# Kernel tuning notes

Hardware: AMD Instinct MI355X
Metric: run time of the kernel (lower is better)

## Reference

```python
import jax, jax.numpy as jnp
import numpy as np

N_HEADS = 16
D_HEAD = 64
QUERY_DIM = 1024
CONTEXT_DIM = 1024
INNER = N_HEADS * D_HEAD


def setup_inputs() -> dict:
    key = jax.random.key(0)
    ks = jax.random.split(key, 7)
    B, Nq, Nk = 4, 1024, 1024
    x = jax.random.normal(ks[0], (B, Nq, QUERY_DIM), dtype=jnp.float32)
    context = jax.random.normal(ks[1], (B, Nk, CONTEXT_DIM), dtype=jnp.float32)
    s_q = 1.0 / np.sqrt(QUERY_DIM)
    s_c = 1.0 / np.sqrt(CONTEXT_DIM)
    s_i = 1.0 / np.sqrt(INNER)
    Wq = jax.random.uniform(ks[2], (QUERY_DIM, INNER), jnp.float32, -s_q, s_q)
    Wk = jax.random.uniform(ks[3], (CONTEXT_DIM, INNER), jnp.float32, -s_c, s_c)
    Wv = jax.random.uniform(ks[4], (CONTEXT_DIM, INNER), jnp.float32, -s_c, s_c)
    Wo = jax.random.uniform(ks[5], (INNER, QUERY_DIM), jnp.float32, -s_i, s_i)
    bo = jax.random.uniform(ks[6], (QUERY_DIM,), jnp.float32, -s_i, s_i)
    return {"x": x, "context": context, "Wq": Wq, "Wk": Wk, "Wv": Wv, "Wo": Wo, "bo": bo}


def reference(x, context, Wq, Wk, Wv, Wo, bo):
    B, Nq, _ = x.shape
    Nk = context.shape[1]
    scale = D_HEAD ** -0.5
    # project and split heads: [B, H, N, d]
    q = (x @ Wq).reshape(B, Nq, N_HEADS, D_HEAD).transpose(0, 2, 1, 3)
    k = (context @ Wk).reshape(B, Nk, N_HEADS, D_HEAD).transpose(0, 2, 1, 3)
    v = (context @ Wv).reshape(B, Nk, N_HEADS, D_HEAD).transpose(0, 2, 1, 3)
    scores = jnp.einsum("bhqd,bhkd->bhqk", q, k) * scale
    attn = jax.nn.softmax(scores, axis=-1)
    out = jnp.einsum("bhqk,bhkd->bhqd", attn, v)
    out = out.transpose(0, 2, 1, 3).reshape(B, Nq, INNER)
    return out @ Wo + bo
```

## Files before the change

### kernel.cpp

```cpp
#include <hip/hip_runtime.h>
#include <hip/hip_bf16.h>

#define BATCH 4
#define NQ 1024
#define NKK 1024
#define HD 1024
#define NHEADS 16

typedef __bf16 bf16x8 __attribute__((ext_vector_type(8)));
typedef float f32x4 __attribute__((ext_vector_type(4)));
typedef unsigned short u16;
typedef unsigned int u32;

__device__ __forceinline__ u16 f2bf(float f) {
    union { __bf16 h; u16 u; } v;
    v.h = (__bf16)f;
    return v.u;
}

#define GLOAD16(gp, lp) \
    __builtin_amdgcn_global_load_lds((const __attribute__((address_space(1))) void*)(gp), \
                                     (__attribute__((address_space(3))) void*)(lp), 16, 0, 0)

#define MFMA16(a, b, c) __builtin_amdgcn_mfma_f32_16x16x32_bf16(a, b, c, 0, 0, 0)

__global__ __launch_bounds__(256) void cvt2bf_k(const float* __restrict__ a,
                                                u16* __restrict__ o, int n4) {
    int i = blockIdx.x * blockDim.x + threadIdx.x;
    const int stride = gridDim.x * blockDim.x;
    for (; i < n4; i += stride) {
        float4 v = ((const float4*)a)[i];
        ushort4 p;
        p.x = f2bf(v.x); p.y = f2bf(v.y); p.z = f2bf(v.z); p.w = f2bf(v.w);
        ((ushort4*)o)[i] = p;
    }
}

__global__ __launch_bounds__(256) void transpose4_k(const float* __restrict__ w0,
                                                    const float* __restrict__ w1,
                                                    const float* __restrict__ w2,
                                                    const float* __restrict__ w3,
                                                    u16* __restrict__ ws) {
    const float* src = blockIdx.z == 0 ? w0 : blockIdx.z == 1 ? w1 : blockIdx.z == 2 ? w2 : w3;
    const float scl = (blockIdx.z == 0) ? 0.18033688011112042f : 1.0f;
    u16* dst = ws + (size_t)blockIdx.z * (1024u * 1024u);
    __shared__ u16 t[64][65];
    const int bx = blockIdx.x * 64;
    const int by = blockIdx.y * 64;
    const int tid = threadIdx.x;
#pragma unroll
    for (int p = 0; p < 16; ++p) {
        int idx = p * 256 + tid;
        int r = idx >> 6, c = idx & 63;
        t[c][r] = f2bf(scl * src[(size_t)(by + r) * 1024 + bx + c]);
    }
    __syncthreads();
#pragma unroll
    for (int p = 0; p < 16; ++p) {
        int idx = p * 256 + tid;
        int r = idx >> 6, c = idx & 63;
        dst[(size_t)(bx + r) * 1024 + by + c] = t[r][c];
    }
}

__global__ __launch_bounds__(256) void gemm_qkv(const u16* __restrict__ Xb,
                                                const u16* __restrict__ Cb,
                                                const u16* __restrict__ WqT,
                                                const u16* __restrict__ WkT,
                                                const u16* __restrict__ WvT,
                                                u16* __restrict__ Qb,
                                                u16* __restrict__ Kb,
                                                u16* __restrict__ VTb) {
    const int bid = blockIdx.x;
    const int swz = (bid & 7) * 192 + (bid >> 3);
    const int z = swz / 512;
    const int rem = swz - z * 512;
    const int m0 = (rem >> 3) * 64;
    const int n0 = (rem & 7) * 128;

    const u16* __restrict__ A  = (z == 0) ? Xb : Cb;
    const u16* __restrict__ BT = (z == 0) ? WqT : (z == 1) ? WkT : WvT;

    __shared__ __align__(16) u16 Asm[64 * 64];
    __shared__ __align__(16) u16 Bsm[128 * 64];

    const int tid = threadIdx.x, lane = tid & 63, wv = tid >> 6;
    const int wm = wv >> 1, wn = wv & 1;
    const int lr = lane & 15, lg = lane >> 4;
    const int lx = lr & 7;
    const int M = BATCH * NQ, N = HD, K = HD;

    f32x4 acc[2][4];
#pragma unroll
    for (int i = 0; i < 2; ++i)
#pragma unroll
        for (int j = 0; j < 4; ++j) acc[i][j] = (f32x4)(0.0f);

    for (int kt = 0; kt < K; kt += 64) {
        __syncthreads();
#pragma unroll
        for (int i = 0; i < 2; ++i) {
            const int cb = (wv * 2 + i) * 64;
            const int s = cb + lane;
            const int row = s >> 3, cg = (s & 7) ^ (row & 7);
            GLOAD16(A + (size_t)(m0 + row) * K + kt + cg * 8, &Asm[cb * 8]);
        }
#pragma unroll
        for (int i = 0; i < 4; ++i) {
            const int cb = (wv * 4 + i) * 64;
            const int s = cb + lane;
            const int row = s >> 3, cg = (s & 7) ^ (row & 7);
            GLOAD16(BT + (size_t)(n0 + row) * K + kt + cg * 8, &Bsm[cb * 8]);
        }
        __syncthreads();
        bf16x8 af[2][2], bfr[4][2];
#pragma unroll
        for (int m = 0; m < 2; ++m)
#pragma unroll
            for (int kk = 0; kk < 2; ++kk)
                af[m][kk] = *(const bf16x8*)&Asm[((wm * 32 + m * 16 + lr) * 8 +
                                                 ((kk * 4 + lg) ^ lx)) * 8];
#pragma unroll
        for (int n = 0; n < 4; ++n)
#pragma unroll
            for (int kk = 0; kk < 2; ++kk)
                bfr[n][kk] = *(const bf16x8*)&Bsm[((wn * 64 + n * 16 + lr) * 8 +
                                                  ((kk * 4 + lg) ^ lx)) * 8];
#pragma unroll
        for (int kk = 0; kk < 2; ++kk)
#pragma unroll
            for (int m = 0; m < 2; ++m)
#pragma unroll
                for (int n = 0; n < 4; ++n)
                    acc[m][n] = MFMA16(af[m][kk], bfr[n][kk], acc[m][n]);
    }

    if (z < 2) {
        u16* __restrict__ C = (z == 0) ? Qb : Kb;
#pragma unroll
        for (int m = 0; m < 2; ++m)
#pragma unroll
            for (int n = 0; n < 4; ++n) {
                const int col = n0 + wn * 64 + n * 16 + lr;
                const int rb = m0 + wm * 32 + m * 16 + lg * 4;
#pragma unroll
                for (int r = 0; r < 4; ++r)
                    C[(size_t)(rb + r) * N + col] = f2bf(acc[m][n][r]);
            }
    } else {
#pragma unroll
        for (int m = 0; m < 2; ++m)
#pragma unroll
            for (int n = 0; n < 4; ++n) {
                const int col = n0 + wn * 64 + n * 16 + lr;
                const int rb = m0 + wm * 32 + m * 16 + lg * 4;
                ushort4 pk;
                pk.x = f2bf(acc[m][n][0]);
                pk.y = f2bf(acc[m][n][1]);
                pk.z = f2bf(acc[m][n][2]);
                pk.w = f2bf(acc[m][n][3]);
                *(ushort4*)&VTb[(size_t)col * M + rb] = pk;
            }
    }
}

__global__ __launch_bounds__(256) void gemm_out(const u16* __restrict__ A,
                                                const u16* __restrict__ BT,
                                                const float* __restrict__ bias,
                                                float* __restrict__ C) {
    const int bid = blockIdx.x;
    const int swz = (bid & 7) * 64 + (bid >> 3);
    const int m0 = (swz >> 3) * 64;
    const int n0 = (swz & 7) * 128;

    __shared__ __align__(16) u16 Asm[64 * 64];
    __shared__ __align__(16) u16 Bsm[128 * 64];

    const int tid = threadIdx.x, lane = tid & 63, wv = tid >> 6;
    const int wm = wv >> 1, wn = wv & 1;
    const int lr = lane & 15, lg = lane >> 4;
    const int lx = lr & 7;
    const int N = HD, K = HD;

    f32x4 acc[2][4];
#pragma unroll
    for (int i = 0; i < 2; ++i)
#pragma unroll
        for (int j = 0; j < 4; ++j) acc[i][j] = (f32x4)(0.0f);

    for (int kt = 0; kt < K; kt += 64) {
        __syncthreads();
#pragma unroll
        for (int i = 0; i < 2; ++i) {
            const int cb = (wv * 2 + i) * 64;
            const int s = cb + lane;
            const int row = s >> 3, cg = (s & 7) ^ (row & 7);
            GLOAD16(A + (size_t)(m0 + row) * K + kt + cg * 8, &Asm[cb * 8]);
        }
#pragma unroll
        for (int i = 0; i < 4; ++i) {
            const int cb = (wv * 4 + i) * 64;
            const int s = cb + lane;
            const int row = s >> 3, cg = (s & 7) ^ (row & 7);
            GLOAD16(BT + (size_t)(n0 + row) * K + kt + cg * 8, &Bsm[cb * 8]);
        }
        __syncthreads();
        bf16x8 af[2][2], bfr[4][2];
#pragma unroll
        for (int m = 0; m < 2; ++m)
#pragma unroll
            for (int kk = 0; kk < 2; ++kk)
                af[m][kk] = *(const bf16x8*)&Asm[((wm * 32 + m * 16 + lr) * 8 +
                                                 ((kk * 4 + lg) ^ lx)) * 8];
#pragma unroll
        for (int n = 0; n < 4; ++n)
#pragma unroll
            for (int kk = 0; kk < 2; ++kk)
                bfr[n][kk] = *(const bf16x8*)&Bsm[((wn * 64 + n * 16 + lr) * 8 +
                                                  ((kk * 4 + lg) ^ lx)) * 8];
#pragma unroll
        for (int kk = 0; kk < 2; ++kk)
#pragma unroll
            for (int m = 0; m < 2; ++m)
#pragma unroll
                for (int n = 0; n < 4; ++n)
                    acc[m][n] = MFMA16(af[m][kk], bfr[n][kk], acc[m][n]);
    }

#pragma unroll
    for (int m = 0; m < 2; ++m)
#pragma unroll
        for (int n = 0; n < 4; ++n) {
            const int col = n0 + wn * 64 + n * 16 + lr;
            const int rb = m0 + wm * 32 + m * 16 + lg * 4;
            const float bv = bias[col];
#pragma unroll
            for (int r = 0; r < 4; ++r)
                C[(size_t)(rb + r) * N + col] = acc[m][n][r] + bv;
        }
}

__global__ __launch_bounds__(256) void attn_k(const u16* __restrict__ Q,
                                              const u16* __restrict__ Kp,
                                              const u16* __restrict__ VT,
                                              u16* __restrict__ AO) {
    __shared__ __align__(16) u16 Ksm[2][64 * 64];
    __shared__ __align__(16) u16 Vsm[2][64 * 64];
    __shared__ __align__(16) u16 Psm[4][16 * 64];

    const int tid = threadIdx.x, lane = tid & 63, wv = tid >> 6;
    const int lr = lane & 15, lg = lane >> 4;

    const int swz = (blockIdx.x & 7) * 128 + (blockIdx.x >> 3);
    const int bh = swz >> 4;
    const int b = bh >> 4, h = bh & 15;
    const int q0 = (swz & 15) * 64 + wv * 16;
    const int lx = lr & 7;

    bf16x8 qf[2];
#pragma unroll
    for (int ks = 0; ks < 2; ++ks)
        qf[ks] = *(const bf16x8*)&Q[(size_t)(b * NQ + q0 + lr) * HD +
                                    h * 64 + ks * 32 + lg * 8];

    const int kbase = b * NKK, vrow0 = h * 64;
    auto stageKV = [&](int kt, int bufsel) {
#pragma unroll
        for (int i = 0; i < 2; ++i) {
            const int cb = (wv * 2 + i) * 64;
            const int s = cb + lane;
            const int row = s >> 3;
            const int cg = (s & 7) ^ (row & 7);
            GLOAD16(Kp + (size_t)(kbase + kt + row) * HD + h * 64 + cg * 8,
                    &Ksm[bufsel][cb * 8]);
            GLOAD16(VT + (size_t)(vrow0 + row) * (BATCH * NKK) + kbase + kt + cg * 8,
                    &Vsm[bufsel][cb * 8]);
        }
    };

    float sum = 0.0f;
    f32x4 o[4];
#pragma unroll
    for (int n = 0; n < 4; ++n) o[n] = (f32x4)(0.0f);

    stageKV(0, 0);
    __syncthreads();
    int cur = 0;

    for (int t = 0; t < NKK / 64; ++t) {
        if (t + 1 < NKK / 64) stageKV((t + 1) * 64, cur ^ 1);
        const u16* Ks = &Ksm[cur][0];
        const u16* Vs = &Vsm[cur][0];

        f32x4 s[4];
#pragma unroll
        for (int n = 0; n < 4; ++n) s[n] = (f32x4)(0.0f);
        __builtin_amdgcn_s_setprio(1);
#pragma unroll
        for (int n = 0; n < 4; ++n) {
            bf16x8 kf0 = *(const bf16x8*)&Ks[(n * 16 + lr) * 64 + (lg ^ lx) * 8];
            bf16x8 kf1 = *(const bf16x8*)&Ks[(n * 16 + lr) * 64 + ((lg | 4) ^ lx) * 8];
            s[n] = MFMA16(kf0, qf[0], s[n]);
            s[n] = MFMA16(kf1, qf[1], s[n]);
        }
        __builtin_amdgcn_s_setprio(0);

        u16* P = &Psm[wv][0];
#pragma unroll
        for (int n = 0; n < 4; ++n) {
            const float p0 = exp2f(s[n][0]);
            const float p1 = exp2f(s[n][1]);
            const float p2 = exp2f(s[n][2]);
            const float p3 = exp2f(s[n][3]);
            sum += (p0 + p1) + (p2 + p3);
            ushort4 pk;
            pk.x = f2bf(p0); pk.y = f2bf(p1); pk.z = f2bf(p2); pk.w = f2bf(p3);
            const int ch = (2 * n + (lg >> 1)) ^ lx;
            *(ushort4*)&P[lr * 64 + ch * 8 + (lg & 1) * 4] = pk;
        }

#pragma unroll
        for (int ks = 0; ks < 2; ++ks) {
            bf16x8 pa = *(const bf16x8*)&P[lr * 64 + (((ks * 4 + lg) ^ lx)) * 8];
            __builtin_amdgcn_s_setprio(1);
#pragma unroll
            for (int n = 0; n < 4; ++n) {
                bf16x8 vf = *(const bf16x8*)&Vs[(n * 16 + lr) * 64 + (((ks * 4 + lg) ^ lx)) * 8];
                o[n] = MFMA16(pa, vf, o[n]);
            }
            __builtin_amdgcn_s_setprio(0);
        }
        __syncthreads();
        cur ^= 1;
    }

    float v = sum;
    v += __shfl_xor(v, 16);
    v += __shfl_xor(v, 32);
    float rs[4];
#pragma unroll
    for (int r = 0; r < 4; ++r)
        rs[r] = 1.0f / __shfl(v, lg * 4 + r);

#pragma unroll
    for (int n = 0; n < 4; ++n)
#pragma unroll
        for (int r = 0; r < 4; ++r) {
            const float val = o[n][r] * rs[r];
            AO[(size_t)(b * NQ + q0 + lg * 4 + r) * HD +
               h * 64 + n * 16 + lr] = f2bf(val);
        }
}

extern "C" void kernel_launch(void* const* d_in, const int* in_sizes, int n_in,
                              void* d_out, int out_size, void* d_ws, size_t ws_size,
                              hipStream_t stream) {
    const float* x   = (const float*)d_in[0];
    const float* ctx = (const float*)d_in[1];
    const float* Wq  = (const float*)d_in[2];
    const float* Wk  = (const float*)d_in[3];
    const float* Wv  = (const float*)d_in[4];
    const float* Wo  = (const float*)d_in[5];
    const float* bo  = (const float*)d_in[6];

    u16* ws = (u16*)d_ws;
    const size_t MEG = 1024u * 1024u;
    u16* WqT = ws + 0 * MEG;
    u16* WkT = ws + 1 * MEG;
    u16* WvT = ws + 2 * MEG;
    u16* WoT = ws + 3 * MEG;
    u16* Xb  = ws + 4 * MEG;
    u16* Cb  = ws + 8 * MEG;
    u16* Qb  = ws + 12 * MEG;
    u16* Kb  = ws + 16 * MEG;
    u16* VTb = ws + 20 * MEG;
    u16* AOb = Xb;

    transpose4_k<<<dim3(16, 16, 4), 256, 0, stream>>>(Wq, Wk, Wv, Wo, ws);
    cvt2bf_k<<<4096, 256, 0, stream>>>(x,   Xb, 1024 * 1024);
    cvt2bf_k<<<4096, 256, 0, stream>>>(ctx, Cb, 1024 * 1024);
    gemm_qkv<<<1536, 256, 0, stream>>>(Xb, Cb, WqT, WkT, WvT, Qb, Kb, VTb);
    attn_k<<<1024, 256, 0, stream>>>(Qb, Kb, VTb, AOb);
    gemm_out<<<512, 256, 0, stream>>>(AOb, WoT, bo, (float*)d_out);
}
```

Baseline: 106.3 us.

## Double-buffer LDS tiles in QKV projection GEMM with async prefetch

Turns the single-buffered LDS staging in the QKV projection GEMM into a two-stage ring. The tile two steps ahead is prefetched via global_load_lds while MFMAs run on the current buffer. Manual vmcnt/lgkmcnt waits and raw barriers replace the per-iteration double __syncthreads, and s_setprio raises priority around the MFMA block. This is meant to hide global load latency, at the cost of doubled LDS use, which may reduce occupancy, and hand-counted waitcnts that must stay exact.

New measurement: 105.5 us. No clear change (-0.8%).

```diff
diff --git a/kernel.cpp b/kernel.cpp
--- a/kernel.cpp
+++ b/kernel.cpp
@@ -81,51 +81,65 @@
     const u16* __restrict__ A  = (z == 0) ? Xb : Cb;
     const u16* __restrict__ BT = (z == 0) ? WqT : (z == 1) ? WkT : WvT;
 
-    __shared__ __align__(16) u16 Asm[64 * 64];
-    __shared__ __align__(16) u16 Bsm[128 * 64];
+    __shared__ __align__(16) u16 Asm[2][64 * 64];
+    __shared__ __align__(16) u16 Bsm[2][128 * 64];
 
     const int tid = threadIdx.x, lane = tid & 63, wv = tid >> 6;
     const int wm = wv >> 1, wn = wv & 1;
     const int lr = lane & 15, lg = lane >> 4;
     const int lx = lr & 7;
     const int M = BATCH * NQ, N = HD, K = HD;
-
-    f32x4 acc[2][4];
-#pragma unroll
-    for (int i = 0; i < 2; ++i)
-#pragma unroll
-        for (int j = 0; j < 4; ++j) acc[i][j] = (f32x4)(0.0f);
-
-    for (int kt = 0; kt < K; kt += 64) {
-        __syncthreads();
+    const int NT = K / 64;
+
+    auto stage = [&](int kt, int bs) {
 #pragma unroll
         for (int i = 0; i < 2; ++i) {
             const int cb = (wv * 2 + i) * 64;
             const int s = cb + lane;
             const int row = s >> 3, cg = (s & 7) ^ (row & 7);
-            GLOAD16(A + (size_t)(m0 + row) * K + kt + cg * 8, &Asm[cb * 8]);
+            GLOAD16(A + (size_t)(m0 + row) * K + kt + cg * 8, &Asm[bs][cb * 8]);
         }
 #pragma unroll
         for (int i = 0; i < 4; ++i) {
             const int cb = (wv * 4 + i) * 64;
             const int s = cb + lane;
             const int row = s >> 3, cg = (s & 7) ^ (row & 7);
-            GLOAD16(BT + (size_t)(n0 + row) * K + kt + cg * 8, &Bsm[cb * 8]);
-        }
-        __syncthreads();
+            GLOAD16(BT + (size_t)(n0 + row) * K + kt + cg * 8, &Bsm[bs][cb * 8]);
+        }
+    };
+
+    f32x4 acc[2][4];
+#pragma unroll
+    for (int i = 0; i < 2; ++i)
+#pragma unroll
+        for (int j = 0; j < 4; ++j) acc[i][j] = (f32x4)(0.0f);
+
+    stage(0, 0);
+    stage(64, 1);
+    asm volatile("s_waitcnt vmcnt(6)" ::: "memory");
+    __builtin_amdgcn_s_barrier();
+
+    for (int t = 0; t < NT; ++t) {
+        const int cb = t & 1;
         bf16x8 af[2][2], bfr[4][2];
 #pragma unroll
         for (int m = 0; m < 2; ++m)
 #pragma unroll
             for (int kk = 0; kk < 2; ++kk)
-                af[m][kk] = *(const bf16x8*)&Asm[((wm * 32 + m * 16 + lr) * 8 +
-                                                 ((kk * 4 + lg) ^ lx)) * 8];
+                af[m][kk] = *(const bf16x8*)&Asm[cb][((wm * 32 + m * 16 + lr) * 8 +
+                                                     ((kk * 4 + lg) ^ lx)) * 8];
 #pragma unroll
         for (int n = 0; n < 4; ++n)
 #pragma unroll
             for (int kk = 0; kk < 2; ++kk)
-                bfr[n][kk] = *(const bf16x8*)&Bsm[((wn * 64 + n * 16 + lr) * 8 +
-                                                  ((kk * 4 + lg) ^ lx)) * 8];
+                bfr[n][kk] = *(const bf16x8*)&Bsm[cb][((wn * 64 + n * 16 + lr) * 8 +
+                                                      ((kk * 4 + lg) ^ lx)) * 8];
+        asm volatile("s_waitcnt lgkmcnt(0)" ::: "memory");
+        __builtin_amdgcn_sched_barrier(0);
+        __builtin_amdgcn_s_barrier();
+        if (t + 2 < NT) stage((t + 2) * 64, cb);
+
+        __builtin_amdgcn_s_setprio(1);
 #pragma unroll
         for (int kk = 0; kk < 2; ++kk)
 #pragma unroll
@@ -133,6 +147,13 @@
 #pragma unroll
                 for (int n = 0; n < 4; ++n)
                     acc[m][n] = MFMA16(af[m][kk], bfr[n][kk], acc[m][n]);
+        __builtin_amdgcn_s_setprio(0);
+
+        if (t + 1 < NT) {
+            if (t + 2 < NT) asm volatile("s_waitcnt vmcnt(6)" ::: "memory");
+            else            asm volatile("s_waitcnt vmcnt(0)" ::: "memory");
+            __builtin_amdgcn_s_barrier();
+        }
     }
 
     if (z < 2) {
```
